# Kernel tuning notes

Measured on AMD Instinct MI355X. Metric: run time of the kernel, lower is better.

## Reference

```python
import jax, jax.numpy as jnp
import numpy as np

N_NODES = 100000
N_EDGES = 1600000
NODE_F = 128
EDGE_F = 64
OUT = 32
NEG_SLOPE = 0.01  # torch nn.LeakyReLU default


def setup_inputs() -> dict:
    key = jax.random.key(0)
    ks = jax.random.split(key, 7)
    h = jax.random.normal(ks[0], (N_NODES, NODE_F), dtype=jnp.float32)
    edge_feat = jax.random.normal(ks[1], (N_EDGES, EDGE_F), dtype=jnp.float32)
    src = jax.random.randint(ks[2], (N_EDGES,), 0, N_NODES)
    dst = jax.random.randint(ks[3], (N_EDGES,), 0, N_NODES)
    W_node = jax.random.normal(ks[4], (NODE_F, OUT), dtype=jnp.float32) * 0.05
    W_edge = jax.random.normal(ks[5], (EDGE_F, OUT), dtype=jnp.float32) * 0.05
    attn_w = jax.random.normal(ks[6], (3 * OUT,), dtype=jnp.float32) * 0.05
    return {"h": h, "edge_feat": edge_feat, "src": src, "dst": dst,
            "W_node": W_node, "W_edge": W_edge, "attn_w": attn_w}


def reference(h, edge_feat, src, dst, W_node, W_edge, attn_w):
    # Project node and edge features (bias-free linears).
    z = h @ W_node                      # [N, OUT]
    ez = edge_feat @ W_edge             # [E, OUT]

    # attn_fc on cat(src_z, dst_z, edge_z): split weight vector to avoid
    # materializing the [E, 3*OUT] concat.
    a_src, a_dst, a_edge = attn_w[:OUT], attn_w[OUT:2 * OUT], attn_w[2 * OUT:]
    zs = z[src]                         # [E, OUT] gather
    logits = jax.nn.leaky_relu(
        zs @ a_src + z[dst] @ a_dst + ez @ a_edge, NEG_SLOPE)  # [E]

    # Per-destination (segment) softmax over incoming edges.
    seg_max = jax.ops.segment_max(logits, dst, num_segments=N_NODES)
    seg_max = jnp.where(jnp.isfinite(seg_max), seg_max, 0.0)  # empty segments
    e = jnp.exp(logits - seg_max[dst])                          # [E]
    denom = jax.ops.segment_sum(e, dst, num_segments=N_NODES)  # [N]

    # Weighted sum of src z vectors per destination.
    num = jax.ops.segment_sum(e[:, None] * zs, dst, num_segments=N_NODES)
    u = num / jnp.maximum(denom, 1e-20)[:, None]                # [N, OUT]
    return u
```

## Files before the change

kernel.cpp:

```cpp
#include <hip/hip_runtime.h>
#include <hip/hip_bf16.h>

#define N_NODES 100000
#define N_EDGES 1600000
#define NODE_F 128
#define EDGE_F 64
#define OUT_F 32
#define NEG_SLOPE 0.01f

__device__ __forceinline__ unsigned short f2bf(float f) {
    unsigned u = __float_as_uint(f);
    unsigned r = u + 0x7fffu + ((u >> 16) & 1u);
    return (unsigned short)(r >> 16);
}
__device__ __forceinline__ float bf2f(unsigned short b) {
    return __uint_as_float((unsigned)b << 16);
}

__global__ void k_node_proj(const float* __restrict__ h,
                            const float* __restrict__ W_node,
                            const float* __restrict__ attn_w,
                            unsigned short* __restrict__ zb,
                            float* __restrict__ s_src,
                            float* __restrict__ s_dst) {
    __shared__ float Ws[NODE_F * OUT_F];
    for (int i = threadIdx.x; i < NODE_F * OUT_F; i += 256)
        Ws[i] = W_node[i];
    __syncthreads();

    int node = blockIdx.x * 8 + (threadIdx.x >> 5);
    int o = threadIdx.x & 31;
    if (node >= N_NODES) return;

    const float* hrow = h + (size_t)node * NODE_F;
    float acc = 0.f;
#pragma unroll 8
    for (int j = 0; j < NODE_F; ++j)
        acc += hrow[j] * Ws[j * OUT_F + o];

    zb[(size_t)node * OUT_F + o] = f2bf(acc);

    float ps = acc * attn_w[o];
    float pd = acc * attn_w[OUT_F + o];
#pragma unroll
    for (int m = 16; m >= 1; m >>= 1) {
        ps += __shfl_xor(ps, m);
        pd += __shfl_xor(pd, m);
    }
    if (o == 0) {
        s_src[node] = ps;
        s_dst[node] = pd;
    }
}

__global__ void k_edge_dot(const float* __restrict__ edge_feat,
                           const int* __restrict__ dst,
                           const float* __restrict__ W_edge,
                           const float* __restrict__ attn_w,
                           float* __restrict__ g,
                           int* __restrict__ deg) {
    __shared__ float we_s[EDGE_F];
    if (threadIdx.x < EDGE_F) {
        float a = 0.f;
#pragma unroll
        for (int kk = 0; kk < OUT_F; ++kk)
            a += W_edge[threadIdx.x * OUT_F + kk] * attn_w[2 * OUT_F + kk];
        we_s[threadIdx.x] = a;
    }
    __syncthreads();

    int t = blockIdx.x * 256 + threadIdx.x;
    int e = t >> 2;
    int sub = t & 3;
    if (e >= N_EDGES) return;

    const float4* row = (const float4*)(edge_feat + (size_t)e * EDGE_F);
    float acc = 0.f;
#pragma unroll
    for (int i = 0; i < 4; ++i) {
        int fi = sub + i * 4;
        float4 v = row[fi];
        int b = fi * 4;
        acc += v.x * we_s[b] + v.y * we_s[b + 1] + v.z * we_s[b + 2] + v.w * we_s[b + 3];
    }
    acc += __shfl_xor(acc, 1);
    acc += __shfl_xor(acc, 2);

    if (sub == 0) {
        g[e] = acc;
        atomicAdd(deg + dst[e], 1);
    }
}

__global__ void k_scan_block(const int* __restrict__ deg,
                             int* __restrict__ offs,
                             int* __restrict__ bsum) {
    __shared__ int wsum[4];
    int i = blockIdx.x * 256 + threadIdx.x;
    int lane = threadIdx.x & 63;
    int wid = threadIdx.x >> 6;
    int v = (i < N_NODES) ? deg[i] : 0;
    int x = v;
#pragma unroll
    for (int d = 1; d < 64; d <<= 1) {
        int y = __shfl_up(x, d);
        if (lane >= d) x += y;
    }
    if (lane == 63) wsum[wid] = x;
    __syncthreads();
    int add = 0;
    for (int w = 0; w < wid; ++w) add += wsum[w];
    int incl = x + add;
    if (i < N_NODES) offs[i] = incl - v;
    if (threadIdx.x == 255) bsum[blockIdx.x] = incl;
}

__global__ void k_scan_bsums(int* __restrict__ bsum, int nb) {
    __shared__ int wsum[8];
    int t = threadIdx.x;
    int lane = t & 63;
    int wid = t >> 6;
    int v = (t < nb) ? bsum[t] : 0;
    int x = v;
#pragma unroll
    for (int d = 1; d < 64; d <<= 1) {
        int y = __shfl_up(x, d);
        if (lane >= d) x += y;
    }
    if (lane == 63) wsum[wid] = x;
    __syncthreads();
    int add = 0;
    for (int w = 0; w < wid; ++w) add += wsum[w];
    int incl = x + add;
    if (t < nb) bsum[t] = incl - v;
}

__global__ void k_scan_add(int* __restrict__ offs,
                           const int* __restrict__ bsum,
                           int* __restrict__ cursor) {
    int i = blockIdx.x * 256 + threadIdx.x;
    if (i < N_NODES) {
        int o = offs[i] + bsum[blockIdx.x];
        offs[i] = o;
        cursor[i] = o;
    }
}

__global__ void k_scatter(const int* __restrict__ src,
                          const int* __restrict__ dst,
                          const float* __restrict__ g,
                          const float* __restrict__ s_src,
                          const float* __restrict__ s_dst,
                          int* __restrict__ cursor,
                          int2* __restrict__ perm) {
    int e = blockIdx.x * 256 + threadIdx.x;
    if (e >= N_EDGES) return;
    int s = src[e], d = dst[e];
    float logit = s_src[s] + s_dst[d] + g[e];
    logit = logit > 0.f ? logit : NEG_SLOPE * logit;
    float ev = __expf(logit);
    int pos = atomicAdd(cursor + d, 1);
    perm[pos] = make_int2(s, __float_as_int(ev));
}

__global__ void k_node_aggr(const int* __restrict__ offs,
                            const int* __restrict__ cursor,
                            const int2* __restrict__ perm,
                            const unsigned short* __restrict__ zb,
                            float* __restrict__ out) {
    int node = blockIdx.x * 8 + (threadIdx.x >> 5);
    int k = threadIdx.x & 31;
    if (node >= N_NODES) return;

    int start = offs[node];
    int end = cursor[node];

    float acc = 0.f, den_local = 0.f;
    for (int base = start; base < end; base += 32) {
        int idx = base + k;
        int cnt = min(32, end - base);
        float ev = 0.f;
        int sp = 0;
        if (idx < end) {
            int2 pr = perm[idx];
            sp = pr.x;
            ev = __int_as_float(pr.y);
        }
        den_local += ev;
        int j = 0;
        for (; j + 4 <= cnt; j += 4) {
            float e0 = __shfl(ev, j, 32), e1 = __shfl(ev, j + 1, 32);
            float e2 = __shfl(ev, j + 2, 32), e3 = __shfl(ev, j + 3, 32);
            int s0 = __shfl(sp, j, 32), s1 = __shfl(sp, j + 1, 32);
            int s2 = __shfl(sp, j + 2, 32), s3 = __shfl(sp, j + 3, 32);
            float z0 = bf2f(zb[(size_t)s0 * OUT_F + k]);
            float z1 = bf2f(zb[(size_t)s1 * OUT_F + k]);
            float z2 = bf2f(zb[(size_t)s2 * OUT_F + k]);
            float z3 = bf2f(zb[(size_t)s3 * OUT_F + k]);
            acc += e0 * z0;
            acc += e1 * z1;
            acc += e2 * z2;
            acc += e3 * z3;
        }
        for (; j < cnt; ++j) {
            float evj = __shfl(ev, j, 32);
            int sj = __shfl(sp, j, 32);
            acc += evj * bf2f(zb[(size_t)sj * OUT_F + k]);
        }
    }

    float den = den_local;
#pragma unroll
    for (int msk = 16; msk >= 1; msk >>= 1)
        den += __shfl_xor(den, msk, 32);

    out[(size_t)node * OUT_F + k] =
        (end > start) ? acc / fmaxf(den, 1e-20f) : 0.f;
}

extern "C" void kernel_launch(void* const* d_in, const int* in_sizes, int n_in,
                              void* d_out, int out_size, void* d_ws, size_t ws_size,
                              hipStream_t stream) {
    const float* h         = (const float*)d_in[0];
    const float* edge_feat = (const float*)d_in[1];
    const int*   src       = (const int*)d_in[2];
    const int*   dst       = (const int*)d_in[3];
    const float* W_node    = (const float*)d_in[4];
    const float* W_edge    = (const float*)d_in[5];
    const float* attn_w    = (const float*)d_in[6];
    float* out = (float*)d_out;

    char* ws = (char*)d_ws;
    size_t off = 0;
    auto alloc = [&](size_t bytes) {
        void* p = ws + off;
        off += (bytes + 255) & ~(size_t)255;
        return p;
    };
    unsigned short* zb = (unsigned short*)alloc((size_t)N_NODES * OUT_F * sizeof(unsigned short));
    float* s_src  = (float*)alloc((size_t)N_NODES * sizeof(float));
    float* s_dst  = (float*)alloc((size_t)N_NODES * sizeof(float));
    float* g      = (float*)alloc((size_t)N_EDGES * sizeof(float));
    int*   deg    = (int*)alloc((size_t)N_NODES * sizeof(int));
    int*   offs   = (int*)alloc((size_t)N_NODES * sizeof(int));
    int*   cursor = (int*)alloc((size_t)N_NODES * sizeof(int));
    int*   bsum   = (int*)alloc(1024 * sizeof(int));
    int2*  perm   = (int2*)alloc((size_t)N_EDGES * sizeof(int2));

    const int NB = (N_NODES + 255) / 256;

    hipMemsetAsync(deg, 0, (size_t)N_NODES * sizeof(int), stream);

    k_node_proj<<<(N_NODES + 7) / 8, 256, 0, stream>>>(h, W_node, attn_w, zb, s_src, s_dst);

    {
        int total = N_EDGES * 4;
        k_edge_dot<<<(total + 255) / 256, 256, 0, stream>>>(edge_feat, dst, W_edge, attn_w, g, deg);
    }
    k_scan_block<<<NB, 256, 0, stream>>>(deg, offs, bsum);
    k_scan_bsums<<<1, 512, 0, stream>>>(bsum, NB);
    k_scan_add<<<NB, 256, 0, stream>>>(offs, bsum, cursor);

    k_scatter<<<(N_EDGES + 255) / 256, 256, 0, stream>>>(
        src, dst, g, s_src, s_dst, cursor, perm);

    k_node_aggr<<<(N_NODES + 7) / 8, 256, 0, stream>>>(
        offs, cursor, perm, zb, out);
}
```

Baseline: 291.3 us.

## Replace three-kernel scan with single-pass decoupled lookback scan and fold memset

Replaces the block-scan, block-sum scan and add kernels with one decoupled-lookback scan kernel that uses dynamic block ids and per-block status words. It also folds the degree-array memset and the scan-state reset into the node projection kernel. The aim is to cut kernel launches and the dependent passes over the degree and offset arrays. In exchange it adds serial spin-waiting on predecessor blocks and relaxed-ordering atomics, and the chain-forward lookback could be slow or subtly racy.

```diff
diff --git a/kernel.cpp b/kernel.cpp
--- a/kernel.cpp
+++ b/kernel.cpp
@@ -7,6 +7,7 @@
 #define EDGE_F 64
 #define OUT_F 32
 #define NEG_SLOPE 0.01f
+#define NB_SCAN 391
 
 __device__ __forceinline__ unsigned short f2bf(float f) {
     unsigned u = __float_as_uint(f);
@@ -22,7 +23,13 @@
                             const float* __restrict__ attn_w,
                             unsigned short* __restrict__ zb,
                             float* __restrict__ s_src,
-                            float* __restrict__ s_dst) {
+                            float* __restrict__ s_dst,
+                            int* __restrict__ deg,
+                            unsigned long long* __restrict__ scan_state) {
+    int gid = blockIdx.x * 256 + threadIdx.x;
+    if (gid < N_NODES) deg[gid] = 0;
+    if (gid <= NB_SCAN) scan_state[gid] = 0ull;
+
     __shared__ float Ws[NODE_F * OUT_F];
     for (int i = threadIdx.x; i < NODE_F * OUT_F; i += 256)
         Ws[i] = W_node[i];
@@ -92,11 +99,21 @@
     }
 }
 
-__global__ void k_scan_block(const int* __restrict__ deg,
-                             int* __restrict__ offs,
-                             int* __restrict__ bsum) {
+__global__ __launch_bounds__(256) void k_scan_lookback(
+    const int* __restrict__ deg,
+    int* __restrict__ offs,
+    int* __restrict__ cursor,
+    unsigned long long* __restrict__ scan_state) {
     __shared__ int wsum[4];
-    int i = blockIdx.x * 256 + threadIdx.x;
+    __shared__ int bid_s;
+    __shared__ int exc_s;
+
+    if (threadIdx.x == 0)
+        bid_s = atomicAdd((unsigned int*)&scan_state[NB_SCAN], 1u);
+    __syncthreads();
+    int bid = bid_s;
+
+    int i = bid * 256 + threadIdx.x;
     int lane = threadIdx.x & 63;
     int wid = threadIdx.x >> 6;
     int v = (i < N_NODES) ? deg[i] : 0;
@@ -111,36 +128,36 @@
     int add = 0;
     for (int w = 0; w < wid; ++w) add += wsum[w];
     int incl = x + add;
-    if (i < N_NODES) offs[i] = incl - v;
-    if (threadIdx.x == 255) bsum[blockIdx.x] = incl;
-}
-
-__global__ void k_scan_bsums(int* __restrict__ bsum, int nb) {
-    __shared__ int wsum[8];
-    int t = threadIdx.x;
-    int lane = t & 63;
-    int wid = t >> 6;
-    int v = (t < nb) ? bsum[t] : 0;
-    int x = v;
-#pragma unroll
-    for (int d = 1; d < 64; d <<= 1) {
-        int y = __shfl_up(x, d);
-        if (lane >= d) x += y;
-    }
-    if (lane == 63) wsum[wid] = x;
-    __syncthreads();
-    int add = 0;
-    for (int w = 0; w < wid; ++w) add += wsum[w];
-    int incl = x + add;
-    if (t < nb) bsum[t] = incl - v;
-}
-
-__global__ void k_scan_add(int* __restrict__ offs,
-                           const int* __restrict__ bsum,
-                           int* __restrict__ cursor) {
-    int i = blockIdx.x * 256 + threadIdx.x;
+
+    if (threadIdx.x == 0) {
+        int bsum = wsum[0] + wsum[1] + wsum[2] + wsum[3];
+        if (bid == 0) {
+            __hip_atomic_store(&scan_state[0], (2ull << 32) | (unsigned)bsum,
+                               __ATOMIC_RELAXED, __HIP_MEMORY_SCOPE_AGENT);
+            exc_s = 0;
+        } else {
+            __hip_atomic_store(&scan_state[bid], (1ull << 32) | (unsigned)bsum,
+                               __ATOMIC_RELAXED, __HIP_MEMORY_SCOPE_AGENT);
+            int pre = 0;
+            for (int j = bid - 1; j >= 0; --j) {
+                unsigned long long s;
+                do {
+                    s = __hip_atomic_load(&scan_state[j], __ATOMIC_RELAXED,
+                                          __HIP_MEMORY_SCOPE_AGENT);
+                } while ((s >> 32) == 0ull);
+                pre += (int)(unsigned)s;
+                if ((s >> 32) == 2ull) break;
+            }
+            __hip_atomic_store(&scan_state[bid],
+                               (2ull << 32) | (unsigned)(pre + bsum),
+                               __ATOMIC_RELAXED, __HIP_MEMORY_SCOPE_AGENT);
+            exc_s = pre;
+        }
+    }
+    __syncthreads();
+
     if (i < N_NODES) {
-        int o = offs[i] + bsum[blockIdx.x];
+        int o = exc_s + incl - v;
         offs[i] = o;
         cursor[i] = o;
     }
@@ -244,22 +261,19 @@
     int*   deg    = (int*)alloc((size_t)N_NODES * sizeof(int));
     int*   offs   = (int*)alloc((size_t)N_NODES * sizeof(int));
     int*   cursor = (int*)alloc((size_t)N_NODES * sizeof(int));
-    int*   bsum   = (int*)alloc(1024 * sizeof(int));
+    unsigned long long* scan_state =
+        (unsigned long long*)alloc((NB_SCAN + 1) * sizeof(unsigned long long));
     int2*  perm   = (int2*)alloc((size_t)N_EDGES * sizeof(int2));
 
-    const int NB = (N_NODES + 255) / 256;
-
-    hipMemsetAsync(deg, 0, (size_t)N_NODES * sizeof(int), stream);
-
-    k_node_proj<<<(N_NODES + 7) / 8, 256, 0, stream>>>(h, W_node, attn_w, zb, s_src, s_dst);
+    k_node_proj<<<(N_NODES + 7) / 8, 256, 0, stream>>>(
+        h, W_node, attn_w, zb, s_src, s_dst, deg, scan_state);
 
     {
         int total = N_EDGES * 4;
         k_edge_dot<<<(total + 255) / 256, 256, 0, stream>>>(edge_feat, dst, W_edge, attn_w, g, deg);
     }
-    k_scan_block<<<NB, 256, 0, stream>>>(deg, offs, bsum);
-    k_scan_bsums<<<1, 512, 0, stream>>>(bsum, NB);
-    k_scan_add<<<NB, 256, 0, stream>>>(offs, bsum, cursor);
+
+    k_scan_lookback<<<NB_SCAN, 256, 0, stream>>>(deg, offs, cursor, scan_state);
 
     k_scatter<<<(N_EDGES + 255) / 256, 256, 0, stream>>>(
         src, dst, g, s_src, s_dst, cursor, perm);
```

Measured after the change: 295.4 us. Within noise of the previous version (+1.4%).
